# Kernel optimization log

Measured on AMD Instinct MI355X. Metric: run time of the kernel, lower is better.

## Reference

```python
import jax, jax.numpy as jnp
import numpy as np

N_NODES = 100000   # graph size
N_EDGES = 1200000  # ~avg degree 12
D_IN = 256
D_OUT = 64


def setup_inputs() -> dict:
    key = jax.random.key(0)
    k1, k2, k3, k4, k5 = jax.random.split(key, 5)
    X = jax.random.normal(k1, (N_NODES, D_IN), dtype=jnp.float32)
    # xavier_uniform-ish scale for W
    limit = np.sqrt(6.0 / (D_IN + D_OUT)).astype(np.float32)
    W = jax.random.uniform(k2, (D_IN, D_OUT), dtype=jnp.float32, minval=-limit, maxval=limit)
    A_rows = jax.random.randint(k3, (N_EDGES,), 0, N_NODES, dtype=jnp.int32)
    A_cols = jax.random.randint(k4, (N_EDGES,), 0, N_NODES, dtype=jnp.int32)
    A_vals = jax.random.uniform(k5, (N_EDGES,), dtype=jnp.float32)  # normalized adjacency weights
    return {"X": X, "W": W, "A_rows": A_rows, "A_cols": A_cols, "A_vals": A_vals}


def reference(X, W, A_rows, A_cols, A_vals) -> jnp.ndarray:
    # support = X @ W  (feature transform; torch.sparse.mm(X, W))
    support = X @ W  # [N, D_OUT]
    # A @ support in COO form: gather source-node features, scale by edge weight,
    # scatter-add into destination rows (torch.sparse.mm(A, support)).
    msgs = A_vals[:, None] * support[A_cols]          # [E, D_OUT]
    out = jax.ops.segment_sum(msgs, A_rows, num_segments=N_NODES)  # [N, D_OUT]
    return out
```

## Files before the change

### kernel.cpp

```cpp
#include <hip/hip_runtime.h>

#define N_NODES 100000
#define N_EDGES 1200000
#define D_IN 256
#define D_OUT 64

#define BUCKET_BITS 5
#define BUCKET_ROWS 32
#define N_BUCKETS   (N_NODES / BUCKET_ROWS)
#define NBLK_E      640
#define EPB         (N_EDGES / NBLK_E)
#define N_GROUPS    196
#define CPL         10
#define CAP         1536

#define C2D_IDX(b, k) ((((size_t)((b) >> 4) * NBLK_E + (k)) << 4) | ((b) & 15))

#define OFF_SUPPORT   0u
#define OFF_BSUM      12800000u
#define OFF_BBASE     12812544u
#define OFF_ETMP      12825088u
#define OFF_EDGEG     22425088u
#define OFF_C2D       OFF_EDGEG
#define WS_NEEDED     32025088u

using bf16x8 = __attribute__((ext_vector_type(8))) short;
using f32x4  = __attribute__((ext_vector_type(4))) float;

static __device__ __forceinline__ ushort f32_to_bf16_rne(float f) {
    unsigned bits = __float_as_uint(f);
    unsigned r = (bits + 0x7FFFu + ((bits >> 16) & 1u)) >> 16;
    return (ushort)r;
}
static __device__ __forceinline__ float bf16_to_f32(ushort u) {
    return __uint_as_float((unsigned)u << 16);
}
static __device__ __forceinline__ unsigned pack2bf(float a, float b) {
    return (unsigned)f32_to_bf16_rne(a) | ((unsigned)f32_to_bf16_rne(b) << 16);
}

__global__ __launch_bounds__(256, 4) void gemm_xw_mfma(const float* __restrict__ X,
                                                       const float* __restrict__ W,
                                                       ushort* __restrict__ support) {
    __shared__ ushort XsT[4][128][8];
    __shared__ ushort WtT[32][64][8];

    const int t = threadIdx.x;
    const int row0 = blockIdx.x * 128;
    const int lane = t & 63;
    const int w = t >> 6;
    const int lr = lane & 15;
    const int lg = lane >> 4;

#pragma unroll
    for (int p = 0; p < 16; ++p) {
        int idx = t + p * 256;
        int k   = idx >> 4;
        int c4  = idx & 15;
        float4 v = *reinterpret_cast<const float4*>(W + (size_t)k * D_OUT + c4 * 4);
        WtT[k >> 3][c4 * 4 + 0][k & 7] = f32_to_bf16_rne(v.x);
        WtT[k >> 3][c4 * 4 + 1][k & 7] = f32_to_bf16_rne(v.y);
        WtT[k >> 3][c4 * 4 + 2][k & 7] = f32_to_bf16_rne(v.z);
        WtT[k >> 3][c4 * 4 + 3][k & 7] = f32_to_bf16_rne(v.w);
    }

    int  xrow[4], xq[4];
    bool xval[4];
#pragma unroll
    for (int p = 0; p < 4; ++p) {
        int idx = t + p * 256;
        xrow[p] = idx >> 3;
        xq[p]   = idx & 7;
        xval[p] = (row0 + xrow[p]) < N_NODES;
    }

    float4 xreg[4];
#pragma unroll
    for (int p = 0; p < 4; ++p) {
        xreg[p] = make_float4(0.f, 0.f, 0.f, 0.f);
        if (xval[p])
            xreg[p] = *reinterpret_cast<const float4*>(
                X + (size_t)(row0 + xrow[p]) * D_IN + xq[p] * 4);
    }

    f32x4 acc[2][4];
#pragma unroll
    for (int mi = 0; mi < 2; ++mi)
#pragma unroll
        for (int ni = 0; ni < 4; ++ni) acc[mi][ni] = (f32x4){0.f, 0.f, 0.f, 0.f};

    for (int kt = 0; kt < 8; ++kt) {
#pragma unroll
        for (int p = 0; p < 4; ++p) {
            uint2 u;
            u.x = pack2bf(xreg[p].x, xreg[p].y);
            u.y = pack2bf(xreg[p].z, xreg[p].w);
            *reinterpret_cast<uint2*>(&XsT[xq[p] >> 1][xrow[p]][(xq[p] & 1) * 4]) = u;
        }
        __syncthreads();

        if (kt < 7) {
#pragma unroll
            for (int p = 0; p < 4; ++p) {
                if (xval[p])
                    xreg[p] = *reinterpret_cast<const float4*>(
                        X + (size_t)(row0 + xrow[p]) * D_IN + (kt + 1) * 32 + xq[p] * 4);
            }
        }

        bf16x8 a0 = *reinterpret_cast<const bf16x8*>(&XsT[lg][w * 32 + lr][0]);
        bf16x8 a1 = *reinterpret_cast<const bf16x8*>(&XsT[lg][w * 32 + 16 + lr][0]);
#pragma unroll
        for (int ni = 0; ni < 4; ++ni) {
            bf16x8 b = *reinterpret_cast<const bf16x8*>(&WtT[kt * 4 + lg][ni * 16 + lr][0]);
            acc[0][ni] = __builtin_amdgcn_mfma_f32_16x16x32_bf16(a0, b, acc[0][ni], 0, 0, 0);
            acc[1][ni] = __builtin_amdgcn_mfma_f32_16x16x32_bf16(a1, b, acc[1][ni], 0, 0, 0);
        }
        __syncthreads();
    }

#pragma unroll
    for (int mi = 0; mi < 2; ++mi) {
#pragma unroll
        for (int reg = 0; reg < 4; ++reg) {
            int grow = row0 + w * 32 + mi * 16 + lg * 4 + reg;
            if (grow < N_NODES) {
#pragma unroll
                for (int ni = 0; ni < 4; ++ni)
                    support[(size_t)grow * D_OUT + ni * 16 + lr] =
                        f32_to_bf16_rne(acc[mi][ni][reg]);
            }
        }
    }
}

__global__ __launch_bounds__(256) void bucket_count(const int* __restrict__ rows,
                                                    int* __restrict__ c2d) {
    __shared__ int h[N_BUCKETS];
    for (int i = threadIdx.x; i < N_BUCKETS; i += 256) h[i] = 0;
    __syncthreads();
    const int base = blockIdx.x * EPB;
    for (int i = threadIdx.x; i < EPB; i += 256)
        atomicAdd(&h[rows[base + i] >> BUCKET_BITS], 1);
    __syncthreads();
    const int k = blockIdx.x;
    for (int b = threadIdx.x; b < N_GROUPS * 16; b += 256)
        c2d[C2D_IDX(b, k)] = (b < N_BUCKETS) ? h[b] : 0;
}

__global__ __launch_bounds__(256) void scan_groups(int* __restrict__ c2d,
                                                   int* __restrict__ bsum) {
    __shared__ int T[16][NBLK_E + 4];
    const int t = threadIdx.x;
    const int w = t >> 6;
    const int l = t & 63;
    const size_t base = (size_t)blockIdx.x * NBLK_E * 16;

    for (int i = t; i < NBLK_E * 16; i += 256) {
        int k = i >> 4, bl = i & 15;
        T[bl][k] = c2d[base + i];
    }
    __syncthreads();

#pragma unroll
    for (int q = 0; q < 4; ++q) {
        const int bl = w * 4 + q;
        int loc[CPL];
        int sum = 0;
#pragma unroll
        for (int j = 0; j < CPL; ++j) {
            int v = T[bl][l * CPL + j];
            loc[j] = sum;
            sum += v;
        }
        int s = sum;
#pragma unroll
        for (int off = 1; off < 64; off <<= 1) {
            int u = __shfl_up(s, off);
            if (l >= off) s += u;
        }
        if (l == 63) bsum[blockIdx.x * 16 + bl] = s;
        int ex = s - sum;
#pragma unroll
        for (int j = 0; j < CPL; ++j)
            T[bl][l * CPL + j] = ex + loc[j];
    }
    __syncthreads();

    for (int i = t; i < NBLK_E * 16; i += 256) {
        int k = i >> 4, bl = i & 15;
        c2d[base + i] = T[bl][k];
    }
}

__global__ __launch_bounds__(256) void scan_buckets(const int* __restrict__ bsum,
                                                    int* __restrict__ bbase) {
    __shared__ int s[256];
    const int t = threadIdx.x;
    int loc[13];
    int sum = 0;
#pragma unroll
    for (int j = 0; j < 13; ++j) {
        int idx = t * 13 + j;
        int v = (idx < N_BUCKETS) ? bsum[idx] : 0;
        loc[j] = sum;
        sum += v;
    }
    s[t] = sum;
    __syncthreads();
#pragma unroll
    for (int off = 1; off < 256; off <<= 1) {
        int x = (t >= off) ? s[t - off] : 0;
        __syncthreads();
        s[t] += x;
        __syncthreads();
    }
    int base = s[t] - sum;
#pragma unroll
    for (int j = 0; j < 13; ++j) {
        int idx = t * 13 + j;
        if (idx < N_BUCKETS) bbase[idx] = base + loc[j];
    }
}

__global__ __launch_bounds__(256) void bucket_scatter2(const int* __restrict__ rows,
                                                       const int* __restrict__ cols,
                                                       const float* __restrict__ vals,
                                                       const int* __restrict__ c2d,
                                                       const int* __restrict__ bbase,
                                                       uint2* __restrict__ etmp) {
    __shared__ int off[N_BUCKETS];
    const int blk = blockIdx.x;
    for (int b = threadIdx.x; b < N_BUCKETS; b += 256)
        off[b] = bbase[b] + c2d[C2D_IDX(b, blk)];
    __syncthreads();
    const int base = blk * EPB;
    for (int i = threadIdx.x; i < EPB; i += 256) {
        int e = base + i;
        int r = rows[e];
        int b = r >> BUCKET_BITS;
        int pos = atomicAdd(&off[b], 1);
        etmp[pos] = make_uint2((unsigned)cols[e] |
                               ((unsigned)(r & (BUCKET_ROWS - 1)) << 17),
                               __float_as_uint(vals[e]));
    }
}

__global__ __launch_bounds__(256) void sort_gather(const uint2* __restrict__ etmp,
                                                   const int* __restrict__ bbase,
                                                   const int* __restrict__ bsum,
                                                   const ushort* __restrict__ support,
                                                   uint2* __restrict__ edge_g,
                                                   float* __restrict__ out) {
    __shared__ uint2 eL[CAP];
    __shared__ int cnt[BUCKET_ROWS], pos[BUCKET_ROWS], fill[BUCKET_ROWS];
    const int t = threadIdx.x;
    const int lane = t & 63;
    const int w = t >> 6;
    const int b = blockIdx.x;
    const int r0 = b << BUCKET_BITS;
    const int s0 = bbase[b];
    const int n  = bsum[b];

    if (t < BUCKET_ROWS) cnt[t] = 0;
    __syncthreads();

    for (int i = t; i < n; i += 256)
        atomicAdd(&cnt[etmp[s0 + i].x >> 17], 1);
    __syncthreads();

    if (t < 64) {
        int v = (t < 32) ? cnt[t] : 0;
        int s = v;
#pragma unroll
        for (int off = 1; off < 32; off <<= 1) {
            int u = __shfl_up(s, off);
            if (lane >= off) s += u;
        }
        if (t < 32) { pos[t] = s - v; fill[t] = 0; }
    }
    __syncthreads();

    const bool inLDS = (n <= CAP);
    if (inLDS) {
        for (int i = t; i < n; i += 256) {
            uint2 u = etmp[s0 + i];
            int r = (int)(u.x >> 17);
            int p = pos[r] + atomicAdd(&fill[r], 1);
            eL[p] = make_uint2(u.x & 0x1FFFFu, u.y);
        }
    } else {
        for (int i = t; i < n; i += 256) {
            uint2 u = etmp[s0 + i];
            int r = (int)(u.x >> 17);
            int p = pos[r] + atomicAdd(&fill[r], 1);
            edge_g[s0 + p] = make_uint2(u.x & 0x1FFFFu, u.y);
        }
    }
    __syncthreads();

    const int h = lane >> 5;
    const int c = lane & 31;

#define GATHER_BODY(SRC)                                                          \
    for (int rr = w; rr < BUCKET_ROWS; rr += 4) {                                 \
        int e = pos[rr], end = pos[rr] + cnt[rr];                                 \
        float2 acc = {0.f, 0.f};                                                  \
        for (; e + 3 < end; e += 4) {                                             \
            uint2 p0 = SRC(e + h);                                                \
            uint2 p1 = SRC(e + 2 + h);                                            \
            unsigned s0v = *reinterpret_cast<const unsigned*>(                    \
                support + (size_t)p0.x * D_OUT + 2 * c);                          \
            unsigned s1v = *reinterpret_cast<const unsigned*>(                    \
                support + (size_t)p1.x * D_OUT + 2 * c);                          \
            float v0 = __uint_as_float(p0.y);                                     \
            float v1 = __uint_as_float(p1.y);                                     \
            acc.x = fmaf(v0, bf16_to_f32((ushort)(s0v & 0xFFFFu)), acc.x);        \
            acc.y = fmaf(v0, bf16_to_f32((ushort)(s0v >> 16)), acc.y);            \
            acc.x = fmaf(v1, bf16_to_f32((ushort)(s1v & 0xFFFFu)), acc.x);        \
            acc.y = fmaf(v1, bf16_to_f32((ushort)(s1v >> 16)), acc.y);            \
        }                                                                         \
        for (int ee = e + h; ee < end; ee += 2) {                                 \
            uint2 p = SRC(ee);                                                    \
            unsigned sv = *reinterpret_cast<const unsigned*>(                     \
                support + (size_t)p.x * D_OUT + 2 * c);                           \
            float v = __uint_as_float(p.y);                                       \
            acc.x = fmaf(v, bf16_to_f32((ushort)(sv & 0xFFFFu)), acc.x);          \
            acc.y = fmaf(v, bf16_to_f32((ushort)(sv >> 16)), acc.y);              \
        }                                                                         \
        acc.x += __shfl_xor(acc.x, 32);                                           \
        acc.y += __shfl_xor(acc.y, 32);                                           \
        if (h == 0)                                                               \
            *reinterpret_cast<float2*>(out + (size_t)(r0 + rr) * D_OUT + 2 * c) = acc; \
    }

    if (inLDS) {
#define SRCL(i) eL[i]
        GATHER_BODY(SRCL)
#undef SRCL
    } else {
        const uint2* eg = edge_g + s0;
#define SRCG(i) eg[i]
        GATHER_BODY(SRCG)
#undef SRCG
    }
#undef GATHER_BODY
}

__global__ void zero_out(float4* __restrict__ out, int n4) {
    int i = blockIdx.x * blockDim.x + threadIdx.x;
    int stride = gridDim.x * blockDim.x;
    for (; i < n4; i += stride) out[i] = float4{0.0f, 0.0f, 0.0f, 0.0f};
}

__global__ __launch_bounds__(256) void spmm_scatter(const int* __restrict__ rows,
                                                    const int* __restrict__ cols,
                                                    const float* __restrict__ vals,
                                                    const ushort* __restrict__ support,
                                                    float* __restrict__ out,
                                                    int n_edges) {
    const int lane = threadIdx.x & 63;
    const int wave_global = (int)((blockIdx.x * blockDim.x + threadIdx.x) >> 6);
    const int n_waves = (int)((gridDim.x * blockDim.x) >> 6);

    for (int base = wave_global * 64; base < n_edges; base += n_waves * 64) {
        int my_e = base + lane;
        int r = rows[my_e];
        int c = cols[my_e];
        float v = vals[my_e];

        int cnt = min(64, n_edges - base);
        for (int i = 0; i < cnt; ++i) {
            int row = __shfl(r, i);
            int col = __shfl(c, i);
            float val = __shfl(v, i);
            float s = bf16_to_f32(support[(size_t)col * D_OUT + lane]);
            atomicAdd(&out[(size_t)row * D_OUT + lane], val * s);
        }
    }
}

extern "C" void kernel_launch(void* const* d_in, const int* in_sizes, int n_in,
                              void* d_out, int out_size, void* d_ws, size_t ws_size,
                              hipStream_t stream) {
    const float* X      = (const float*)d_in[0];
    const float* W      = (const float*)d_in[1];
    const int*   A_rows = (const int*)d_in[2];
    const int*   A_cols = (const int*)d_in[3];
    const float* A_vals = (const float*)d_in[4];
    float* out = (float*)d_out;

    char* ws = (char*)d_ws;
    ushort* support = (ushort*)(ws + OFF_SUPPORT);

    const int gemm_blocks = (N_NODES + 127) / 128;

    if (ws_size >= (size_t)WS_NEEDED) {
        int*   bsum   = (int*)(ws + OFF_BSUM);
        int*   bbase  = (int*)(ws + OFF_BBASE);
        int*   c2d    = (int*)(ws + OFF_C2D);
        uint2* etmp   = (uint2*)(ws + OFF_ETMP);
        uint2* edge_g = (uint2*)(ws + OFF_EDGEG);

        bucket_count<<<NBLK_E, 256, 0, stream>>>(A_rows, c2d);
        scan_groups<<<N_GROUPS, 256, 0, stream>>>(c2d, bsum);
        scan_buckets<<<1, 256, 0, stream>>>(bsum, bbase);

        bucket_scatter2<<<NBLK_E, 256, 0, stream>>>(A_rows, A_cols, A_vals,
                                                    c2d, bbase, etmp);

        gemm_xw_mfma<<<gemm_blocks, 256, 0, stream>>>(X, W, support);

        sort_gather<<<N_BUCKETS, 256, 0, stream>>>(etmp, bbase, bsum,
                                                   support, edge_g, out);
    } else {
        int n4 = (N_NODES * D_OUT) / 4;
        zero_out<<<2048, 256, 0, stream>>>((float4*)out, n4);
        gemm_xw_mfma<<<gemm_blocks, 256, 0, stream>>>(X, W, support);
        int chunks = N_EDGES / 64;
        spmm_scatter<<<(chunks + 3) / 4, 256, 0, stream>>>(A_rows, A_cols, A_vals,
                                                           support, out, N_EDGES);
    }
}
```

Baseline: 103.6 us.

## Split GEMM blocks across preprocessing launches to overlap with bucketing stages

The X@W GEMM blocks are spread across three merged launches (250, 200 and 332 blocks, 782 in total). Each launch also runs one bucket-sort preprocessing stage: count, bucket scan, or scatter. This fills idle compute units during the latency-bound sort stages and removes a separate GEMM launch. In exchange, every merged launch now reserves 40KB of shared memory per block and uses launch_bounds(256,4), which may lower occupancy for the sort stages.

```diff
diff --git a/kernel.cpp b/kernel.cpp
--- a/kernel.cpp
+++ b/kernel.cpp
@@ -14,6 +14,11 @@
 #define CPL         10
 #define CAP         1536
 
+#define GEMM_BLOCKS 782
+#define GA 250
+#define GB 200
+#define GC 332
+
 #define C2D_IDX(b, k) ((((size_t)((b) >> 4) * NBLK_E + (k)) << 4) | ((b) & 15))
 
 #define OFF_SUPPORT   0u
@@ -39,14 +44,14 @@
     return (unsigned)f32_to_bf16_rne(a) | ((unsigned)f32_to_bf16_rne(b) << 16);
 }
 
-__global__ __launch_bounds__(256, 4) void gemm_xw_mfma(const float* __restrict__ X,
-                                                       const float* __restrict__ W,
-                                                       ushort* __restrict__ support) {
-    __shared__ ushort XsT[4][128][8];
-    __shared__ ushort WtT[32][64][8];
+static __device__ void gemm_role(int row0, char* smem,
+                                 const float* __restrict__ X,
+                                 const float* __restrict__ W,
+                                 ushort* __restrict__ support) {
+    auto XsT = reinterpret_cast<ushort(*)[128][8]>(smem);
+    auto WtT = reinterpret_cast<ushort(*)[64][8]>(smem + 8192);
 
     const int t = threadIdx.x;
-    const int row0 = blockIdx.x * 128;
     const int lane = t & 63;
     const int w = t >> 6;
     const int lr = lane & 15;
@@ -134,18 +139,78 @@
     }
 }
 
-__global__ __launch_bounds__(256) void bucket_count(const int* __restrict__ rows,
-                                                    int* __restrict__ c2d) {
-    __shared__ int h[N_BUCKETS];
-    for (int i = threadIdx.x; i < N_BUCKETS; i += 256) h[i] = 0;
-    __syncthreads();
-    const int base = blockIdx.x * EPB;
-    for (int i = threadIdx.x; i < EPB; i += 256)
-        atomicAdd(&h[rows[base + i] >> BUCKET_BITS], 1);
-    __syncthreads();
-    const int k = blockIdx.x;
-    for (int b = threadIdx.x; b < N_GROUPS * 16; b += 256)
-        c2d[C2D_IDX(b, k)] = (b < N_BUCKETS) ? h[b] : 0;
+__global__ __launch_bounds__(256, 4) void mega(int stage, int n_other, int gemm_base,
+                                               const float* __restrict__ X,
+                                               const float* __restrict__ W,
+                                               ushort* __restrict__ support,
+                                               const int* __restrict__ rows,
+                                               const int* __restrict__ cols,
+                                               const float* __restrict__ vals,
+                                               int* __restrict__ c2d,
+                                               const int* __restrict__ bsum,
+                                               int* __restrict__ bbase,
+                                               uint2* __restrict__ etmp) {
+    __shared__ __align__(16) char smem[40960];
+    const int bid = blockIdx.x;
+    const int t = threadIdx.x;
+
+    if (bid >= n_other) {
+        gemm_role((gemm_base + bid - n_other) * 128, smem, X, W, support);
+        return;
+    }
+
+    if (stage == 0) {
+        int* h = reinterpret_cast<int*>(smem);
+        for (int i = t; i < N_BUCKETS; i += 256) h[i] = 0;
+        __syncthreads();
+        const int base = bid * EPB;
+        for (int i = t; i < EPB; i += 256)
+            atomicAdd(&h[rows[base + i] >> BUCKET_BITS], 1);
+        __syncthreads();
+        for (int b = t; b < N_GROUPS * 16; b += 256)
+            c2d[C2D_IDX(b, bid)] = (b < N_BUCKETS) ? h[b] : 0;
+    } else if (stage == 1) {
+        int* s = reinterpret_cast<int*>(smem);
+        int loc[13];
+        int sum = 0;
+#pragma unroll
+        for (int j = 0; j < 13; ++j) {
+            int idx = t * 13 + j;
+            int v = (idx < N_BUCKETS) ? bsum[idx] : 0;
+            loc[j] = sum;
+            sum += v;
+        }
+        s[t] = sum;
+        __syncthreads();
+#pragma unroll
+        for (int off = 1; off < 256; off <<= 1) {
+            int x = (t >= off) ? s[t - off] : 0;
+            __syncthreads();
+            s[t] += x;
+            __syncthreads();
+        }
+        int base = s[t] - sum;
+#pragma unroll
+        for (int j = 0; j < 13; ++j) {
+            int idx = t * 13 + j;
+            if (idx < N_BUCKETS) bbase[idx] = base + loc[j];
+        }
+    } else {
+        int* off = reinterpret_cast<int*>(smem);
+        for (int b = t; b < N_BUCKETS; b += 256)
+            off[b] = bbase[b] + c2d[C2D_IDX(b, bid)];
+        __syncthreads();
+        const int base = bid * EPB;
+        for (int i = t; i < EPB; i += 256) {
+            int e = base + i;
+            int r = rows[e];
+            int b = r >> BUCKET_BITS;
+            int pos = atomicAdd(&off[b], 1);
+            etmp[pos] = make_uint2((unsigned)cols[e] |
+                                   ((unsigned)(r & (BUCKET_ROWS - 1)) << 17),
+                                   __float_as_uint(vals[e]));
+        }
+    }
 }
 
 __global__ __launch_bounds__(256) void scan_groups(int* __restrict__ c2d,
@@ -190,59 +255,6 @@
     for (int i = t; i < NBLK_E * 16; i += 256) {
         int k = i >> 4, bl = i & 15;
         c2d[base + i] = T[bl][k];
-    }
-}
-
-__global__ __launch_bounds__(256) void scan_buckets(const int* __restrict__ bsum,
-                                                    int* __restrict__ bbase) {
-    __shared__ int s[256];
-    const int t = threadIdx.x;
-    int loc[13];
-    int sum = 0;
-#pragma unroll
-    for (int j = 0; j < 13; ++j) {
-        int idx = t * 13 + j;
-        int v = (idx < N_BUCKETS) ? bsum[idx] : 0;
-        loc[j] = sum;
-        sum += v;
-    }
-    s[t] = sum;
-    __syncthreads();
-#pragma unroll
-    for (int off = 1; off < 256; off <<= 1) {
-        int x = (t >= off) ? s[t - off] : 0;
-        __syncthreads();
-        s[t] += x;
-        __syncthreads();
-    }
-    int base = s[t] - sum;
-#pragma unroll
-    for (int j = 0; j < 13; ++j) {
-        int idx = t * 13 + j;
-        if (idx < N_BUCKETS) bbase[idx] = base + loc[j];
-    }
-}
-
-__global__ __launch_bounds__(256) void bucket_scatter2(const int* __restrict__ rows,
-                                                       const int* __restrict__ cols,
-                                                       const float* __restrict__ vals,
-                                                       const int* __restrict__ c2d,
-                                                       const int* __restrict__ bbase,
-                                                       uint2* __restrict__ etmp) {
-    __shared__ int off[N_BUCKETS];
-    const int blk = blockIdx.x;
-    for (int b = threadIdx.x; b < N_BUCKETS; b += 256)
-        off[b] = bbase[b] + c2d[C2D_IDX(b, blk)];
-    __syncthreads();
-    const int base = blk * EPB;
-    for (int i = threadIdx.x; i < EPB; i += 256) {
-        int e = base + i;
-        int r = rows[e];
-        int b = r >> BUCKET_BITS;
-        int pos = atomicAdd(&off[b], 1);
-        etmp[pos] = make_uint2((unsigned)cols[e] |
-                               ((unsigned)(r & (BUCKET_ROWS - 1)) << 17),
-                               __float_as_uint(vals[e]));
     }
 }
 
@@ -347,6 +359,13 @@
 #undef GATHER_BODY
 }
 
+__global__ __launch_bounds__(256, 4) void gemm_standalone(const float* __restrict__ X,
+                                                          const float* __restrict__ W,
+                                                          ushort* __restrict__ support) {
+    __shared__ __align__(16) char smem[40960];
+    gemm_role(blockIdx.x * 128, smem, X, W, support);
+}
+
 __global__ void zero_out(float4* __restrict__ out, int n4) {
     int i = blockIdx.x * blockDim.x + threadIdx.x;
     int stride = gridDim.x * blockDim.x;
@@ -393,8 +412,6 @@
     char* ws = (char*)d_ws;
     ushort* support = (ushort*)(ws + OFF_SUPPORT);
 
-    const int gemm_blocks = (N_NODES + 127) / 128;
-
     if (ws_size >= (size_t)WS_NEEDED) {
         int*   bsum   = (int*)(ws + OFF_BSUM);
         int*   bbase  = (int*)(ws + OFF_BBASE);
@@ -402,21 +419,22 @@
         uint2* etmp   = (uint2*)(ws + OFF_ETMP);
         uint2* edge_g = (uint2*)(ws + OFF_EDGEG);
 
-        bucket_count<<<NBLK_E, 256, 0, stream>>>(A_rows, c2d);
+        mega<<<NBLK_E + GA, 256, 0, stream>>>(0, NBLK_E, 0, X, W, support,
+                                              A_rows, A_cols, A_vals,
+                                              c2d, bsum, bbase, etmp);
         scan_groups<<<N_GROUPS, 256, 0, stream>>>(c2d, bsum);
-        scan_buckets<<<1, 256, 0, stream>>>(bsum, bbase);
-
-        bucket_scatter2<<<NBLK_E, 256, 0, stream>>>(A_rows, A_cols, A_vals,
-                                                    c2d, bbase, etmp);
-
-        gemm_xw_mfma<<<gemm_blocks, 256, 0, stream>>>(X, W, support);
-
+        mega<<<1 + GB, 256, 0, stream>>>(1, 1, GA, X, W, support,
+                                         A_rows, A_cols, A_vals,
+                                         c2d, bsum, bbase, etmp);
+        mega<<<NBLK_E + GC, 256, 0, stream>>>(2, NBLK_E, GA + GB, X, W, support,
+                                              A_rows, A_cols, A_vals,
+                                              c2d, bsum, bbase, etmp);
         sort_gather<<<N_BUCKETS, 256, 0, stream>>>(etmp, bbase, bsum,
                                                    support, edge_g, out);
     } else {
         int n4 = (N_NODES * D_OUT) / 4;
         zero_out<<<2048, 256, 0, stream>>>((float4*)out, n4);
-        gemm_xw_mfma<<<gemm_blocks, 256, 0, stream>>>(X, W, support);
+        gemm_standalone<<<GEMM_BLOCKS, 256, 0, stream>>>(X, W, support);
         int chunks = N_EDGES / 64;
         spmm_scatter<<<(chunks + 3) / 4, 256, 0, stream>>>(A_rows, A_cols, A_vals,
                                                            support, out, N_EDGES);
```

Measured after the change: 119.0 us. +14.8%, slower.

## Fuse bucket scan into scatter kernel and process two row tiles per GEMM block

Applied to the files above, without the earlier changes.

Removes the single-block scan_buckets launch by having every scatter block redundantly compute the bucket prefix scan itself, with block 0 writing bbase for the later stage. This drops one kernel launch and its serialization point, at the cost of each of the 640 blocks repeating a small 3125-entry scan. Separately, the GEMM now loops over two 128-row tiles per block, halving the block count so the W load and bf16 transpose into shared memory are amortized over more rows, with less parallelism in exchange.

```diff
diff --git a/kernel.cpp b/kernel.cpp
--- a/kernel.cpp
+++ b/kernel.cpp
@@ -46,7 +46,6 @@
     __shared__ ushort WtT[32][64][8];
 
     const int t = threadIdx.x;
-    const int row0 = blockIdx.x * 128;
     const int lane = t & 63;
     const int w = t >> 6;
     const int lr = lane & 15;
@@ -64,71 +63,78 @@
         WtT[k >> 3][c4 * 4 + 3][k & 7] = f32_to_bf16_rne(v.w);
     }
 
-    int  xrow[4], xq[4];
-    bool xval[4];
+    int xrow[4], xq[4];
 #pragma unroll
     for (int p = 0; p < 4; ++p) {
         int idx = t + p * 256;
         xrow[p] = idx >> 3;
         xq[p]   = idx & 7;
-        xval[p] = (row0 + xrow[p]) < N_NODES;
-    }
-
-    float4 xreg[4];
-#pragma unroll
-    for (int p = 0; p < 4; ++p) {
-        xreg[p] = make_float4(0.f, 0.f, 0.f, 0.f);
-        if (xval[p])
-            xreg[p] = *reinterpret_cast<const float4*>(
-                X + (size_t)(row0 + xrow[p]) * D_IN + xq[p] * 4);
-    }
-
-    f32x4 acc[2][4];
-#pragma unroll
-    for (int mi = 0; mi < 2; ++mi)
-#pragma unroll
-        for (int ni = 0; ni < 4; ++ni) acc[mi][ni] = (f32x4){0.f, 0.f, 0.f, 0.f};
-
-    for (int kt = 0; kt < 8; ++kt) {
+    }
+
+    for (int tile = 0; tile < 2; ++tile) {
+        const int row0 = blockIdx.x * 256 + tile * 128;
+        if (row0 >= N_NODES) break;
+
+        bool xval[4];
+#pragma unroll
+        for (int p = 0; p < 4; ++p) xval[p] = (row0 + xrow[p]) < N_NODES;
+
+        float4 xreg[4];
 #pragma unroll
         for (int p = 0; p < 4; ++p) {
-            uint2 u;
-            u.x = pack2bf(xreg[p].x, xreg[p].y);
-            u.y = pack2bf(xreg[p].z, xreg[p].w);
-            *reinterpret_cast<uint2*>(&XsT[xq[p] >> 1][xrow[p]][(xq[p] & 1) * 4]) = u;
-        }
-        __syncthreads();
-
-        if (kt < 7) {
+            xreg[p] = make_float4(0.f, 0.f, 0.f, 0.f);
+            if (xval[p])
+                xreg[p] = *reinterpret_cast<const float4*>(
+                    X + (size_t)(row0 + xrow[p]) * D_IN + xq[p] * 4);
+        }
+
+        f32x4 acc[2][4];
+#pragma unroll
+        for (int mi = 0; mi < 2; ++mi)
+#pragma unroll
+            for (int ni = 0; ni < 4; ++ni) acc[mi][ni] = (f32x4){0.f, 0.f, 0.f, 0.f};
+
+        for (int kt = 0; kt < 8; ++kt) {
 #pragma unroll
             for (int p = 0; p < 4; ++p) {
-                if (xval[p])
-                    xreg[p] = *reinterpret_cast<const float4*>(
-                        X + (size_t)(row0 + xrow[p]) * D_IN + (kt + 1) * 32 + xq[p] * 4);
+                uint2 u;
+                u.x = pack2bf(xreg[p].x, xreg[p].y);
+                u.y = pack2bf(xreg[p].z, xreg[p].w);
+                *reinterpret_cast<uint2*>(&XsT[xq[p] >> 1][xrow[p]][(xq[p] & 1) * 4]) = u;
             }
-        }
-
-        bf16x8 a0 = *reinterpret_cast<const bf16x8*>(&XsT[lg][w * 32 + lr][0]);
-        bf16x8 a1 = *reinterpret_cast<const bf16x8*>(&XsT[lg][w * 32 + 16 + lr][0]);
-#pragma unroll
-        for (int ni = 0; ni < 4; ++ni) {
-            bf16x8 b = *reinterpret_cast<const bf16x8*>(&WtT[kt * 4 + lg][ni * 16 + lr][0]);
-            acc[0][ni] = __builtin_amdgcn_mfma_f32_16x16x32_bf16(a0, b, acc[0][ni], 0, 0, 0);
-            acc[1][ni] = __builtin_amdgcn_mfma_f32_16x16x32_bf16(a1, b, acc[1][ni], 0, 0, 0);
-        }
-        __syncthreads();
-    }
-
-#pragma unroll
-    for (int mi = 0; mi < 2; ++mi) {
-#pragma unroll
-        for (int reg = 0; reg < 4; ++reg) {
-            int grow = row0 + w * 32 + mi * 16 + lg * 4 + reg;
-            if (grow < N_NODES) {
-#pragma unroll
-                for (int ni = 0; ni < 4; ++ni)
-                    support[(size_t)grow * D_OUT + ni * 16 + lr] =
-                        f32_to_bf16_rne(acc[mi][ni][reg]);
+            __syncthreads();
+
+            if (kt < 7) {
+#pragma unroll
+                for (int p = 0; p < 4; ++p) {
+                    if (xval[p])
+                        xreg[p] = *reinterpret_cast<const float4*>(
+                            X + (size_t)(row0 + xrow[p]) * D_IN + (kt + 1) * 32 + xq[p] * 4);
+                }
+            }
+
+            bf16x8 a0 = *reinterpret_cast<const bf16x8*>(&XsT[lg][w * 32 + lr][0]);
+            bf16x8 a1 = *reinterpret_cast<const bf16x8*>(&XsT[lg][w * 32 + 16 + lr][0]);
+#pragma unroll
+            for (int ni = 0; ni < 4; ++ni) {
+                bf16x8 b = *reinterpret_cast<const bf16x8*>(&WtT[kt * 4 + lg][ni * 16 + lr][0]);
+                acc[0][ni] = __builtin_amdgcn_mfma_f32_16x16x32_bf16(a0, b, acc[0][ni], 0, 0, 0);
+                acc[1][ni] = __builtin_amdgcn_mfma_f32_16x16x32_bf16(a1, b, acc[1][ni], 0, 0, 0);
+            }
+            __syncthreads();
+        }
+
+#pragma unroll
+        for (int mi = 0; mi < 2; ++mi) {
+#pragma unroll
+            for (int reg = 0; reg < 4; ++reg) {
+                int grow = row0 + w * 32 + mi * 16 + lg * 4 + reg;
+                if (grow < N_NODES) {
+#pragma unroll
+                    for (int ni = 0; ni < 4; ++ni)
+                        support[(size_t)grow * D_OUT + ni * 16 + lr] =
+                            f32_to_bf16_rne(acc[mi][ni][reg]);
+                }
             }
         }
     }
@@ -193,10 +199,18 @@
     }
 }
 
-__global__ __launch_bounds__(256) void scan_buckets(const int* __restrict__ bsum,
-                                                    int* __restrict__ bbase) {
+__global__ __launch_bounds__(256) void bucket_scatter3(const int* __restrict__ rows,
+                                                       const int* __restrict__ cols,
+                                                       const float* __restrict__ vals,
+                                                       const int* __restrict__ c2d,
+                                                       const int* __restrict__ bsum,
+                                                       int* __restrict__ bbase,
+                                                       uint2* __restrict__ etmp) {
     __shared__ int s[256];
+    __shared__ int off[N_BUCKETS];
     const int t = threadIdx.x;
+    const int blk = blockIdx.x;
+
     int loc[13];
     int sum = 0;
 #pragma unroll
@@ -209,33 +223,26 @@
     s[t] = sum;
     __syncthreads();
 #pragma unroll
-    for (int off = 1; off < 256; off <<= 1) {
-        int x = (t >= off) ? s[t - off] : 0;
+    for (int o = 1; o < 256; o <<= 1) {
+        int x = (t >= o) ? s[t - o] : 0;
         __syncthreads();
         s[t] += x;
         __syncthreads();
     }
-    int base = s[t] - sum;
+    int base0 = s[t] - sum;
 #pragma unroll
     for (int j = 0; j < 13; ++j) {
         int idx = t * 13 + j;
-        if (idx < N_BUCKETS) bbase[idx] = base + loc[j];
-    }
-}
-
-__global__ __launch_bounds__(256) void bucket_scatter2(const int* __restrict__ rows,
-                                                       const int* __restrict__ cols,
-                                                       const float* __restrict__ vals,
-                                                       const int* __restrict__ c2d,
-                                                       const int* __restrict__ bbase,
-                                                       uint2* __restrict__ etmp) {
-    __shared__ int off[N_BUCKETS];
-    const int blk = blockIdx.x;
-    for (int b = threadIdx.x; b < N_BUCKETS; b += 256)
-        off[b] = bbase[b] + c2d[C2D_IDX(b, blk)];
-    __syncthreads();
+        if (idx < N_BUCKETS) {
+            int bb = base0 + loc[j];
+            off[idx] = bb + c2d[C2D_IDX(idx, blk)];
+            if (blk == 0) bbase[idx] = bb;
+        }
+    }
+    __syncthreads();
+
     const int base = blk * EPB;
-    for (int i = threadIdx.x; i < EPB; i += 256) {
+    for (int i = t; i < EPB; i += 256) {
         int e = base + i;
         int r = rows[e];
         int b = r >> BUCKET_BITS;
@@ -393,7 +400,7 @@
     char* ws = (char*)d_ws;
     ushort* support = (ushort*)(ws + OFF_SUPPORT);
 
-    const int gemm_blocks = (N_NODES + 127) / 128;
+    const int gemm_blocks = (N_NODES + 255) / 256;
 
     if (ws_size >= (size_t)WS_NEEDED) {
         int*   bsum   = (int*)(ws + OFF_BSUM);
@@ -404,13 +411,9 @@
 
         bucket_count<<<NBLK_E, 256, 0, stream>>>(A_rows, c2d);
         scan_groups<<<N_GROUPS, 256, 0, stream>>>(c2d, bsum);
-        scan_buckets<<<1, 256, 0, stream>>>(bsum, bbase);
-
-        bucket_scatter2<<<NBLK_E, 256, 0, stream>>>(A_rows, A_cols, A_vals,
-                                                    c2d, bbase, etmp);
-
+        bucket_scatter3<<<NBLK_E, 256, 0, stream>>>(A_rows, A_cols, A_vals,
+                                                    c2d, bsum, bbase, etmp);
         gemm_xw_mfma<<<gemm_blocks, 256, 0, stream>>>(X, W, support);
-
         sort_gather<<<N_BUCKETS, 256, 0, stream>>>(etmp, bbase, bsum,
                                                    support, edge_g, out);
     } else {
```

Result: slower. 111.9 us (+8.0%).
